# Kernel tuning notes

Hardware: AMD Instinct MI355X
Metric: run time of the kernel (lower is better)

## Reference

```python
import jax, jax.numpy as jnp
import numpy as np


def setup_inputs() -> dict:
    key = jax.random.key(0)
    ks = jax.random.split(key, 5)
    b, t, e, h = 8, 1024, 256, 8
    w = lambda k, shape: jax.random.normal(k, shape, dtype=jnp.float32) * 0.02
    return {
        "x": jax.random.normal(ks[0], (b, t, e), dtype=jnp.float32),
        "Wq": w(ks[1], (e, e * h)), "bq": jnp.zeros((e * h,), jnp.float32),
        "Wk": w(ks[2], (e, e * h)), "bk": jnp.zeros((e * h,), jnp.float32),
        "Wv": w(ks[3], (e, e * h)), "bv": jnp.zeros((e * h,), jnp.float32),
        "Wu": w(ks[4], (e * h, e)), "bu": jnp.zeros((e,), jnp.float32),
    }


def reference(x, Wq, bq, Wk, bk, Wv, bv, Wu, bu):
    b, t, e = x.shape
    h = Wq.shape[1] // e  # each head has FULL width e in this module
    q = (x @ Wq + bq).reshape(b, t, h, e)
    k = (x @ Wk + bk).reshape(b, t, h, e)
    v = (x @ Wv + bv).reshape(b, t, h, e)
    # scores: (b, h, t, t), scaled by sqrt(e) as in the original
    scores = jnp.einsum('bihe,bjhe->bhij', q, k) / jnp.sqrt(jnp.asarray(e, jnp.float32))
    i = jnp.arange(t)[:, None]
    j = jnp.arange(t)[None, :]
    # mask mode 'first': triu(offset=0) -> -inf, i.e. query i sees only j < i
    scores = jnp.where(j >= i, -jnp.inf, scores)
    # row 0 is fully masked (torch softmax -> NaN, then zeroed post-softmax);
    # make it finite first so softmax is well-defined, then zero the attention row
    scores = jnp.where(i == 0, 0.0, scores)
    att = jax.nn.softmax(scores, axis=-1)
    att = jnp.where(i == 0, 0.0, att)
    out = jnp.einsum('bhij,bjhe->bihe', att, v).reshape(b, t, h * e)
    return out @ Wu + bu
```

## Files before the change

kernel.cpp:

```cpp
#include <hip/hip_runtime.h>
#include <hip/hip_bf16.h>

typedef unsigned short u16;
typedef short bf16x8 __attribute__((ext_vector_type(8)));
typedef float f32x4 __attribute__((ext_vector_type(4)));

#define EXP2(x) __builtin_amdgcn_exp2f(x)

static __device__ __forceinline__ u16 f2bf(float f) {
  union { float f; unsigned u; } a; a.f = f;
  unsigned r = a.u + 0x7fffu + ((a.u >> 16) & 1u);
  return (u16)(r >> 16);
}

static __device__ __forceinline__ unsigned pkbf(float a, float b) {
  union { __hip_bfloat162 h; unsigned u; } c;
  c.h = __float22bfloat162_rn(make_float2(a, b));
  return c.u;
}

static __device__ __forceinline__ bf16x8 as_bf(int4 v) {
  union { int4 i; bf16x8 b; } u; u.i = v; return u.b;
}

#define GLDS16(g, l)                                         \
  __builtin_amdgcn_global_load_lds(                          \
      (const __attribute__((address_space(1))) void*)(g),    \
      (__attribute__((address_space(3))) void*)(l), 16, 0, 0)

__global__ __launch_bounds__(256) void prep(
    const float* __restrict__ x, u16* __restrict__ Xb,
    const float* __restrict__ Wq, u16* __restrict__ Wqt,
    const float* __restrict__ Wk, u16* __restrict__ Wkt,
    const float* __restrict__ Wv, u16* __restrict__ Wvt,
    const float* __restrict__ Wu, u16* __restrict__ Wut) {
  const int bid = blockIdx.x, tid = threadIdx.x;
  if (bid < 1024) {
    int i = bid * 256 + tid;
    const float4* p = (const float4*)x + (size_t)i * 2;
    float4 a = p[0], b = p[1];
    union { unsigned s[4]; int4 v; } u2;
    u2.s[0] = pkbf(a.x, a.y); u2.s[1] = pkbf(a.z, a.w);
    u2.s[2] = pkbf(b.x, b.y); u2.s[3] = pkbf(b.z, b.w);
    ((int4*)Xb)[i] = u2.v;
    return;
  }
  const int which = (bid - 1024) >> 6;
  const float* in; u16* out; int R, C;
  if (which == 0)      { in = Wq; out = Wqt; R = 256;  C = 2048; }
  else if (which == 1) { in = Wk; out = Wkt; R = 256;  C = 2048; }
  else if (which == 2) { in = Wv; out = Wvt; R = 256;  C = 2048; }
  else                 { in = Wu; out = Wut; R = 2048; C = 256;  }
  int T = ((bid - 1024) & 63) * 256 + tid;
  int c = T % C;
  int r0 = (T / C) * 32;
  __align__(16) u16 tmp[32];
#pragma unroll
  for (int j = 0; j < 32; ++j) tmp[j] = f2bf(in[(size_t)(r0 + j) * C + c]);
#pragma unroll
  for (int q = 0; q < 4; ++q)
    *(int4*)(out + (size_t)c * R + r0 + q * 8) = *(int4*)&tmp[q * 8];
}

__global__ __launch_bounds__(256) void gemm_qkv(const u16* __restrict__ A,
                                                const u16* __restrict__ Wt,
                                                const float* __restrict__ bq,
                                                const float* __restrict__ bk,
                                                const float* __restrict__ bv,
                                                u16* __restrict__ Qw,
                                                u16* __restrict__ Kw,
                                                u16* __restrict__ Vt) {
  constexpr int BM = 128, BN = 128, BK = 64;
  __shared__ int4 smem4[2048];
  int4* As4 = smem4;
  int4* Bs4 = smem4 + 1024;
  const int tid = threadIdx.x;
  const int w = tid >> 6, lane = tid & 63, lq = lane & 15, quad = lane >> 4;
  const int wm = w >> 1, wn = w & 1;
  const int m0 = blockIdx.y * BM, n0 = blockIdx.x * BN;
  const int z = blockIdx.z;

  const u16* Btz = Wt + (size_t)z * 2048 * 256;
  const float* bias = (z == 0) ? bq : (z == 1 ? bk : bv);

  const int srow = lane >> 3;
  const int scb = (lane & 7) ^ ((lane >> 3) & 7);

  f32x4 acc[4][4];
#pragma unroll
  for (int mi = 0; mi < 4; ++mi)
#pragma unroll
    for (int ni = 0; ni < 4; ++ni) {
      f32x4 z4 = {0.f, 0.f, 0.f, 0.f};
      acc[mi][ni] = z4;
    }

  for (int k0 = 0; k0 < 256; k0 += BK) {
    __syncthreads();
#pragma unroll
    for (int it = 0; it < 4; ++it) {
      int r = (w * 4 + it) * 8 + srow;
      GLDS16(A + (size_t)(m0 + r) * 256 + k0 + scb * 8,
             (char*)As4 + (w * 4 + it) * 1024);
    }
#pragma unroll
    for (int it = 0; it < 4; ++it) {
      int r = (w * 4 + it) * 8 + srow;
      GLDS16(Btz + (size_t)(n0 + r) * 256 + k0 + scb * 8,
             (char*)Bs4 + (w * 4 + it) * 1024);
    }
    __syncthreads();
#pragma unroll
    for (int kk = 0; kk < 2; ++kk) {
      int4 af[4], bf[4];
#pragma unroll
      for (int mi = 0; mi < 4; ++mi) {
        int r = wm * 64 + mi * 16 + lq;
        af[mi] = As4[r * 8 + ((kk * 4 + quad) ^ (lq & 7))];
      }
#pragma unroll
      for (int ni = 0; ni < 4; ++ni) {
        int r = wn * 64 + ni * 16 + lq;
        bf[ni] = Bs4[r * 8 + ((kk * 4 + quad) ^ (lq & 7))];
      }
#pragma unroll
      for (int mi = 0; mi < 4; ++mi)
#pragma unroll
        for (int ni = 0; ni < 4; ++ni)
          acc[mi][ni] = __builtin_amdgcn_mfma_f32_16x16x32_bf16(
              as_bf(af[mi]), as_bf(bf[ni]), acc[mi][ni], 0, 0, 0);
    }
  }

  if (z < 2) {
    u16* Cout = z ? Kw : Qw;
#pragma unroll
    for (int mi = 0; mi < 4; ++mi)
#pragma unroll
      for (int ni = 0; ni < 4; ++ni)
#pragma unroll
        for (int r = 0; r < 4; ++r) {
          int row = m0 + wm * 64 + mi * 16 + quad * 4 + r;
          int col = n0 + wn * 64 + ni * 16 + lq;
          Cout[(size_t)row * 2048 + col] = f2bf(acc[mi][ni][r] + bias[col]);
        }
  } else {
    __syncthreads();
    u16* Ts = (u16*)smem4;
#pragma unroll
    for (int mi = 0; mi < 4; ++mi)
#pragma unroll
      for (int ni = 0; ni < 4; ++ni) {
        int c = wn * 64 + ni * 16 + lq;
        int r0 = wm * 64 + mi * 16 + quad * 4;
        float vb = bias[n0 + c];
        uint2 dd;
        dd.x = pkbf(acc[mi][ni][0] + vb, acc[mi][ni][1] + vb);
        dd.y = pkbf(acc[mi][ni][2] + vb, acc[mi][ni][3] + vb);
        *(uint2*)&Ts[c * 128 + (((r0 >> 3) ^ (c & 15)) << 3) + (r0 & 7)] = dd;
      }
    __syncthreads();
    const int b = m0 >> 10, t0 = m0 & 1023;
    const int e0 = n0 & 255, h = n0 >> 8;
    const int bh = b * 8 + h;
    const int i4 = tid & 15;
#pragma unroll
    for (int cc = 0; cc < 8; ++cc) {
      int c = (tid >> 4) + cc * 16;
      int4 val = *(const int4*)&Ts[c * 128 + ((i4 ^ (c & 15)) << 3)];
      *(int4*)(Vt + (size_t)(bh * 256 + e0 + c) * 1024 + t0 + i4 * 8) = val;
    }
  }
}

template <int BM, int BN>
__global__ __launch_bounds__(256) void gemm_bt(const u16* __restrict__ A,
                                               const u16* __restrict__ Bt,
                                               const float* __restrict__ bias,
                                               float* __restrict__ Cout,
                                               int M, int N, int K) {
  constexpr int BK = 64;
  constexpr int TM = BM / 2 / 16, TN = BN / 2 / 16;
  constexpr int nA = BM / 32, nB = BN / 32;
  __shared__ int4 As4[BM * 8];
  __shared__ int4 Bs4[BN * 8];
  const int tid = threadIdx.x;
  const int w = tid >> 6, lane = tid & 63, lq = lane & 15, quad = lane >> 4;
  const int wm = w >> 1, wn = w & 1;
  const int m0 = blockIdx.y * BM, n0 = blockIdx.x * BN;

  const int srow = lane >> 3;
  const int scb = (lane & 7) ^ ((lane >> 3) & 7);

  f32x4 acc[TM][TN];
#pragma unroll
  for (int mi = 0; mi < TM; ++mi)
#pragma unroll
    for (int ni = 0; ni < TN; ++ni) {
      f32x4 z4 = {0.f, 0.f, 0.f, 0.f};
      acc[mi][ni] = z4;
    }

  for (int k0 = 0; k0 < K; k0 += BK) {
    __syncthreads();
#pragma unroll
    for (int it = 0; it < nA; ++it) {
      int r = (w * nA + it) * 8 + srow;
      GLDS16(A + (size_t)(m0 + r) * K + k0 + scb * 8,
             (char*)As4 + (w * nA + it) * 1024);
    }
#pragma unroll
    for (int it = 0; it < nB; ++it) {
      int r = (w * nB + it) * 8 + srow;
      GLDS16(Bt + (size_t)(n0 + r) * K + k0 + scb * 8,
             (char*)Bs4 + (w * nB + it) * 1024);
    }
    __syncthreads();
#pragma unroll
    for (int kk = 0; kk < BK / 32; ++kk) {
      int4 af[TM], bf[TN];
#pragma unroll
      for (int mi = 0; mi < TM; ++mi) {
        int r = wm * (BM / 2) + mi * 16 + lq;
        af[mi] = As4[r * 8 + ((kk * 4 + quad) ^ (lq & 7))];
      }
#pragma unroll
      for (int ni = 0; ni < TN; ++ni) {
        int r = wn * (BN / 2) + ni * 16 + lq;
        bf[ni] = Bs4[r * 8 + ((kk * 4 + quad) ^ (lq & 7))];
      }
#pragma unroll
      for (int mi = 0; mi < TM; ++mi)
#pragma unroll
        for (int ni = 0; ni < TN; ++ni)
          acc[mi][ni] = __builtin_amdgcn_mfma_f32_16x16x32_bf16(
              as_bf(af[mi]), as_bf(bf[ni]), acc[mi][ni], 0, 0, 0);
    }
  }

#pragma unroll
  for (int mi = 0; mi < TM; ++mi)
#pragma unroll
    for (int ni = 0; ni < TN; ++ni)
#pragma unroll
      for (int r = 0; r < 4; ++r) {
        int row = m0 + wm * (BM / 2) + mi * 16 + quad * 4 + r;
        int col = n0 + wn * (BN / 2) + ni * 16 + lq;
        Cout[(size_t)row * N + col] = acc[mi][ni][r] + bias[col];
      }
}

__global__ __launch_bounds__(256, 2) void attn_kernel(const u16* __restrict__ Q,
                                                      const u16* __restrict__ Km,
                                                      const u16* __restrict__ Vt,
                                                      u16* __restrict__ O) {
  const int bh = blockIdx.x;
  const int pair = blockIdx.y;
  const int b = bh >> 3, h = bh & 7;
  const int tid = threadIdx.x;
  const int w = tid >> 6, lane = tid & 63, lq = lane & 15, quad = lane >> 4;

  __shared__ int4 Ks4[2048];
  __shared__ int4 Vs4[2048];
  __shared__ u16 Ps[4096];
  u16* myPs = Ps + w * 1024;

  int koffb[8], voffb[8];
  {
    const int kg = (lane & 31) >> 3;
#pragma unroll
    for (int it = 0; it < 8; ++it) {
      int r = w * 16 + it * 2 + (lane >> 5);
      int p = (lane & 7) ^ (r & 7);
      koffb[it] = r * 2048 + (kg * 8 + p) * 8;
      int rv = w * 64 + it * 8 + (lane >> 3);
      int cb = (lane & 7) ^ (rv & 7);
      voffb[it] = rv * 1024 + cb * 8;
    }
  }
  const u16* kbase = Km + (size_t)b * 2097152 + h * 256;
  const u16* vbase = Vt + (size_t)bh * 262144;

  const float SCL = 0.09016844f;
  const float NEG = -3.0e38f;

#pragma unroll 1
  for (int hv = 0; hv < 2; ++hv) {
    const int qt = hv ? (15 - pair) : pair;
    const int qg = qt * 64 + w * 16 + lq;
    const u16* qptr = Q + (size_t)(b * 1024 + qg) * 2048 + h * 256 + quad * 8;
    int4 qf[8];
#pragma unroll
    for (int kk = 0; kk < 8; ++kk) qf[kk] = *(const int4*)(qptr + kk * 32);

    f32x4 of[16];
#pragma unroll
    for (int i = 0; i < 16; ++i) {
      f32x4 z = {0.f, 0.f, 0.f, 0.f};
      of[i] = z;
    }
    float mst = NEG, lst = 0.f;

    for (int kt = 0; kt <= qt; ++kt) {
      __syncthreads();
      {
        const u16* kb = kbase + (size_t)kt * 131072;
        const u16* vb = vbase + kt * 64;
#pragma unroll
        for (int it = 0; it < 8; ++it)
          GLDS16(kb + koffb[it], (char*)Ks4 + (w * 8 + it) * 1024);
#pragma unroll
        for (int it = 0; it < 8; ++it)
          GLDS16(vb + voffb[it], (char*)Vs4 + (w * 8 + it) * 1024);
      }
      __syncthreads();

      f32x4 sc[4];
#pragma unroll
      for (int ns = 0; ns < 4; ++ns) {
        f32x4 a = {0.f, 0.f, 0.f, 0.f};
        int r = ns * 16 + lq;
#pragma unroll
        for (int kk = 0; kk < 8; ++kk) {
          int G = kk * 4 + quad;
          int4 kf = Ks4[r * 32 + (G >> 3) * 8 + ((G & 7) ^ (lq & 7))];
          a = __builtin_amdgcn_mfma_f32_16x16x32_bf16(as_bf(kf), as_bf(qf[kk]),
                                                      a, 0, 0, 0);
        }
        sc[ns] = a;
      }
#pragma unroll
      for (int ns = 0; ns < 4; ++ns) {
        int keyb = kt * 64 + ns * 16 + quad * 4;
#pragma unroll
        for (int r = 0; r < 4; ++r) {
          float v = sc[ns][r] * SCL;
          sc[ns][r] = (keyb + r >= qg) ? NEG : v;
        }
      }
      float m16 = sc[0][0];
#pragma unroll
      for (int ns = 0; ns < 4; ++ns)
#pragma unroll
        for (int r = 0; r < 4; ++r) m16 = fmaxf(m16, sc[ns][r]);
      m16 = fmaxf(m16, __shfl_xor(m16, 16));
      m16 = fmaxf(m16, __shfl_xor(m16, 32));
      if (__any(m16 > mst)) {
        float mn = fmaxf(mst, m16);
        float alpha = EXP2(mst - mn);
        mst = mn;
        lst *= alpha;
#pragma unroll
        for (int i = 0; i < 16; ++i)
#pragma unroll
          for (int r = 0; r < 4; ++r) of[i][r] *= alpha;
      }
      float s = 0.f;
#pragma unroll
      for (int ns = 0; ns < 4; ++ns)
#pragma unroll
        for (int r = 0; r < 4; ++r) {
          float p = EXP2(sc[ns][r] - mst);
          sc[ns][r] = p;
          s += p;
        }
      s += __shfl_xor(s, 16);
      s += __shfl_xor(s, 32);
      lst += s;

#pragma unroll
      for (int ns = 0; ns < 4; ++ns) {
        int kb2 = ns * 2 + (quad >> 1);
        int base = lq * 64 + ((kb2 ^ (lq & 7)) << 3) + (quad & 1) * 4;
        *(unsigned*)&myPs[base] = pkbf(sc[ns][0], sc[ns][1]);
        *(unsigned*)&myPs[base + 2] = pkbf(sc[ns][2], sc[ns][3]);
      }
      int4 pf[2];
#pragma unroll
      for (int kk2 = 0; kk2 < 2; ++kk2) {
        int kbp = (kk2 * 4 + quad) ^ (lq & 7);
        pf[kk2] = *(const int4*)&myPs[lq * 64 + kbp * 8];
      }
#pragma unroll
      for (int ns2 = 0; ns2 < 16; ++ns2) {
        int r = ns2 * 16 + lq;
#pragma unroll
        for (int kk2 = 0; kk2 < 2; ++kk2) {
          int4 vf = Vs4[r * 8 + ((kk2 * 4 + quad) ^ (lq & 7))];
          of[ns2] = __builtin_amdgcn_mfma_f32_16x16x32_bf16(
              as_bf(vf), as_bf(pf[kk2]), of[ns2], 0, 0, 0);
        }
      }
    }

    float inv = lst > 0.f ? 1.f / lst : 0.f;
    if (qg == 0) inv = 0.f;
    u16* optr = O + (size_t)(b * 1024 + qg) * 2048 + h * 256 + quad * 4;
#pragma unroll
    for (int ns2 = 0; ns2 < 16; ++ns2) {
      uint2 o4;
      o4.x = pkbf(of[ns2][0] * inv, of[ns2][1] * inv);
      o4.y = pkbf(of[ns2][2] * inv, of[ns2][3] * inv);
      *(uint2*)(optr + ns2 * 16) = o4;
    }
  }
}

#define WS_XB 0
#define WS_WQT 4194304
#define WS_WUT 7340032
#define WS_QW 8388608
#define WS_KW 41943040
#define WS_OW 75497472
#define WS_VTW 109051904

extern "C" void kernel_launch(void* const* d_in, const int* in_sizes, int n_in,
                              void* d_out, int out_size, void* d_ws, size_t ws_size,
                              hipStream_t stream) {
  const float* x = (const float*)d_in[0];
  const float* Wq = (const float*)d_in[1];
  const float* bq = (const float*)d_in[2];
  const float* Wk = (const float*)d_in[3];
  const float* bk = (const float*)d_in[4];
  const float* Wv = (const float*)d_in[5];
  const float* bv = (const float*)d_in[6];
  const float* Wu = (const float*)d_in[7];
  const float* bu = (const float*)d_in[8];
  float* out = (float*)d_out;

  char* ws = (char*)d_ws;
  u16* Xb = (u16*)(ws + WS_XB);
  u16* Wqt = (u16*)(ws + WS_WQT);
  u16* Wkt = Wqt + 524288;
  u16* Wvt = Wqt + 1048576;
  u16* Wut = (u16*)(ws + WS_WUT);
  u16* Qw = (u16*)(ws + WS_QW);
  u16* Kw = (u16*)(ws + WS_KW);
  u16* Ow = (u16*)(ws + WS_OW);
  u16* Vtw = (u16*)(ws + WS_VTW);

  prep<<<1280, 256, 0, stream>>>(x, Xb, Wq, Wqt, Wk, Wkt, Wv, Wvt, Wu, Wut);

  gemm_qkv<<<dim3(16, 64, 3), 256, 0, stream>>>(Xb, Wqt, bq, bk, bv, Qw, Kw, Vtw);

  attn_kernel<<<dim3(64, 8), 256, 0, stream>>>(Qw, Kw, Vtw, Ow);

  gemm_bt<64, 64><<<dim3(4, 128), 256, 0, stream>>>(Ow, Wut, bu, out, 8192, 256, 2048);
}
```

Baseline: 215.9 us.

## Double-buffer K/V tiles with 32-key blocks and MFMA priority hints

```diff
diff --git a/kernel.cpp b/kernel.cpp
--- a/kernel.cpp
+++ b/kernel.cpp
@@ -260,26 +260,38 @@
   const int tid = threadIdx.x;
   const int w = tid >> 6, lane = tid & 63, lq = lane & 15, quad = lane >> 4;
 
-  __shared__ int4 Ks4[2048];
-  __shared__ int4 Vs4[2048];
-  __shared__ u16 Ps[4096];
-  u16* myPs = Ps + w * 1024;
-
-  int koffb[8], voffb[8];
+  __shared__ int4 Ks4[2][1024];
+  __shared__ int4 Vs4[2][1024];
+  __shared__ u16 Ps[2048];
+  u16* myPs = Ps + w * 512;
+
+  int koffb[4], voffb[4];
   {
     const int kg = (lane & 31) >> 3;
 #pragma unroll
-    for (int it = 0; it < 8; ++it) {
-      int r = w * 16 + it * 2 + (lane >> 5);
+    for (int it = 0; it < 4; ++it) {
+      int j = w * 4 + it;
+      int r = j * 2 + (lane >> 5);
       int p = (lane & 7) ^ (r & 7);
       koffb[it] = r * 2048 + (kg * 8 + p) * 8;
-      int rv = w * 64 + it * 8 + (lane >> 3);
-      int cb = (lane & 7) ^ (rv & 7);
+      int rv = j * 16 + (lane >> 2);
+      int cb = (lane & 3) ^ ((rv >> 1) & 3);
       voffb[it] = rv * 1024 + cb * 8;
     }
   }
   const u16* kbase = Km + (size_t)b * 2097152 + h * 256;
   const u16* vbase = Vt + (size_t)bh * 262144;
+
+  auto STAGE = [&](int bs, int kt) {
+    const u16* kb = kbase + (size_t)kt * 65536;
+    const u16* vb = vbase + kt * 32;
+#pragma unroll
+    for (int it = 0; it < 4; ++it)
+      GLDS16(kb + koffb[it], (char*)&Ks4[bs][0] + (w * 4 + it) * 1024);
+#pragma unroll
+    for (int it = 0; it < 4; ++it)
+      GLDS16(vb + voffb[it], (char*)&Vs4[bs][0] + (w * 4 + it) * 1024);
+  };
 
   const float SCL = 0.09016844f;
   const float NEG = -3.0e38f;
@@ -301,37 +313,33 @@
     }
     float mst = NEG, lst = 0.f;
 
-    for (int kt = 0; kt <= qt; ++kt) {
-      __syncthreads();
-      {
-        const u16* kb = kbase + (size_t)kt * 131072;
-        const u16* vb = vbase + kt * 64;
-#pragma unroll
-        for (int it = 0; it < 8; ++it)
-          GLDS16(kb + koffb[it], (char*)Ks4 + (w * 8 + it) * 1024);
-#pragma unroll
-        for (int it = 0; it < 8; ++it)
-          GLDS16(vb + voffb[it], (char*)Vs4 + (w * 8 + it) * 1024);
-      }
-      __syncthreads();
-
-      f32x4 sc[4];
-#pragma unroll
-      for (int ns = 0; ns < 4; ++ns) {
+    const int kmax = 2 * qt + 1;
+    STAGE(0, 0);
+    __syncthreads();
+    int buf = 0;
+
+    for (int kt = 0; kt <= kmax; ++kt) {
+      if (kt < kmax) STAGE(buf ^ 1, kt + 1);
+
+      f32x4 sc[2];
+      __builtin_amdgcn_s_setprio(1);
+#pragma unroll
+      for (int ns = 0; ns < 2; ++ns) {
         f32x4 a = {0.f, 0.f, 0.f, 0.f};
         int r = ns * 16 + lq;
 #pragma unroll
         for (int kk = 0; kk < 8; ++kk) {
           int G = kk * 4 + quad;
-          int4 kf = Ks4[r * 32 + (G >> 3) * 8 + ((G & 7) ^ (lq & 7))];
+          int4 kf = Ks4[buf][r * 32 + (G >> 3) * 8 + ((G & 7) ^ (lq & 7))];
           a = __builtin_amdgcn_mfma_f32_16x16x32_bf16(as_bf(kf), as_bf(qf[kk]),
                                                       a, 0, 0, 0);
         }
         sc[ns] = a;
       }
-#pragma unroll
-      for (int ns = 0; ns < 4; ++ns) {
-        int keyb = kt * 64 + ns * 16 + quad * 4;
+      __builtin_amdgcn_s_setprio(0);
+#pragma unroll
+      for (int ns = 0; ns < 2; ++ns) {
+        int keyb = kt * 32 + ns * 16 + quad * 4;
 #pragma unroll
         for (int r = 0; r < 4; ++r) {
           float v = sc[ns][r] * SCL;
@@ -340,7 +348,7 @@
       }
       float m16 = sc[0][0];
 #pragma unroll
-      for (int ns = 0; ns < 4; ++ns)
+      for (int ns = 0; ns < 2; ++ns)
 #pragma unroll
         for (int r = 0; r < 4; ++r) m16 = fmaxf(m16, sc[ns][r]);
       m16 = fmaxf(m16, __shfl_xor(m16, 16));
@@ -357,7 +365,7 @@
       }
       float s = 0.f;
 #pragma unroll
-      for (int ns = 0; ns < 4; ++ns)
+      for (int ns = 0; ns < 2; ++ns)
 #pragma unroll
         for (int r = 0; r < 4; ++r) {
           float p = EXP2(sc[ns][r] - mst);
@@ -369,28 +377,26 @@
       lst += s;
 
 #pragma unroll
-      for (int ns = 0; ns < 4; ++ns) {
+      for (int ns = 0; ns < 2; ++ns) {
         int kb2 = ns * 2 + (quad >> 1);
-        int base = lq * 64 + ((kb2 ^ (lq & 7)) << 3) + (quad & 1) * 4;
+        int base = lq * 32 + ((kb2 ^ (lq & 3)) << 3) + (quad & 1) * 4;
         *(unsigned*)&myPs[base] = pkbf(sc[ns][0], sc[ns][1]);
         *(unsigned*)&myPs[base + 2] = pkbf(sc[ns][2], sc[ns][3]);
       }
-      int4 pf[2];
-#pragma unroll
-      for (int kk2 = 0; kk2 < 2; ++kk2) {
-        int kbp = (kk2 * 4 + quad) ^ (lq & 7);
-        pf[kk2] = *(const int4*)&myPs[lq * 64 + kbp * 8];
-      }
+      int4 pf = *(const int4*)&myPs[lq * 32 + ((quad ^ (lq & 3)) << 3)];
+
+      __builtin_amdgcn_s_setprio(1);
 #pragma unroll
       for (int ns2 = 0; ns2 < 16; ++ns2) {
-        int r = ns2 * 16 + lq;
-#pragma unroll
-        for (int kk2 = 0; kk2 < 2; ++kk2) {
-          int4 vf = Vs4[r * 8 + ((kk2 * 4 + quad) ^ (lq & 7))];
-          of[ns2] = __builtin_amdgcn_mfma_f32_16x16x32_bf16(
-              as_bf(vf), as_bf(pf[kk2]), of[ns2], 0, 0, 0);
-        }
-      }
+        int rv = ns2 * 16 + lq;
+        int4 vf = Vs4[buf][rv * 4 + (quad ^ ((lq >> 1) & 3))];
+        of[ns2] = __builtin_amdgcn_mfma_f32_16x16x32_bf16(
+            as_bf(vf), as_bf(pf), of[ns2], 0, 0, 0);
+      }
+      __builtin_amdgcn_s_setprio(0);
+
+      __syncthreads();
+      buf ^= 1;
     }
 
     float inv = lst > 0.f ? 1.f / lst : 0.f;
```

After: 227.9 us. 1.06x slower.
